# Kernel optimization log

Measured on AMD Instinct MI355X. Metric: run time of the kernel, lower is better.

Reference implementation:

```python
import jax, jax.numpy as jnp
import numpy as np

N_NODES = 10000
N_EDGES = 160000
DIM = 128
NLAYERS = 3
NBASIS = 16
NSPECIES = 100
CUTOFF = 5.0


def _mlp(x, W1, b1, W2, b2):
    # FullyConnectedNet([hidden, out]) with silu on hidden, linear output
    return jax.nn.silu(x @ W1 + b1) @ W2 + b2


def setup_inputs() -> dict:
    key = jax.random.key(0)
    ks = iter(jax.random.split(key, 64))
    scale = 0.08

    def w(shape):
        return jax.random.normal(next(ks), shape, dtype=jnp.float32) * scale

    inp = {
        "species": jax.random.randint(next(ks), (N_NODES,), 0, NSPECIES, dtype=jnp.int32),
        "edge_src": jnp.sort(jax.random.randint(next(ks), (N_EDGES,), 0, N_NODES, dtype=jnp.int32)),
        "edge_dst": jax.random.randint(next(ks), (N_EDGES,), 0, N_NODES, dtype=jnp.int32),
        "distances": 0.5 + 4.4 * jax.random.uniform(next(ks), (N_EDGES,), dtype=jnp.float32),
        "vec": jax.random.normal(next(ks), (N_EDGES, 3), dtype=jnp.float32),
        "switch": jax.random.uniform(next(ks), (N_EDGES,), dtype=jnp.float32),
        "species_W": w((NSPECIES, DIM)),
        "species_b": w((DIM,)),
        "radial_W": w((NLAYERS, NBASIS, DIM)),
        "radial_b": w((NLAYERS, DIM)),
    }
    for nm, out in [("a", DIM), ("F", 1), ("f", DIM), ("R", DIM), ("r", DIM), ("u", DIM)]:
        inp[nm + "_W1"] = w((NLAYERS, DIM, DIM))
        inp[nm + "_b1"] = w((NLAYERS, DIM))
        inp[nm + "_W2"] = w((NLAYERS, DIM, out))
        inp[nm + "_b2"] = w((NLAYERS, out))
    return inp


def reference(species, edge_src, edge_dst, distances, vec, switch,
              species_W, species_b, radial_W, radial_b,
              a_W1, a_b1, a_W2, a_b2,
              F_W1, F_b1, F_W2, F_b2,
              f_W1, f_b1, f_W2, f_b2,
              R_W1, R_b1, R_W2, R_b2,
              r_W1, r_b1, r_W2, r_b2,
              u_W1, u_b1, u_W2, u_b2):
    N = species.shape[0]
    # species encoding -> species_linear Dense
    xi = jax.nn.one_hot(species, NSPECIES, dtype=jnp.float32) @ species_W + species_b  # (N, dim)
    sw = switch[:, None]                                   # (E, 1)
    dirij = vec / distances[:, None] * sw                  # (E, 3)
    # gaussian radial basis on [0, cutoff]
    centers = jnp.linspace(0.0, CUTOFF, NBASIS, dtype=jnp.float32)
    eta = jnp.float32((NBASIS / CUTOFF) ** 2)
    rb = jnp.exp(-eta * (distances[:, None] - centers) ** 2)  # (E, nbasis)

    fi = None
    di = None
    for l in range(NLAYERS):
        ai = _mlp(xi, a_W1[l], a_b1[l], a_W2[l], a_b2[l])          # (N, dim)
        Dij = rb @ radial_W[l] + radial_b[l]                        # (E, dim)
        mij = ai[edge_src] * ai[edge_dst] * Dij * sw                # (E, dim)
        xi = xi + jax.ops.segment_sum(mij, edge_src, N)
        Fij = _mlp(mij, F_W1[l], F_b1[l], F_W2[l], F_b2[l]) * dirij  # (E, 3)
        fij = _mlp(mij, f_W1[l], f_b1[l], f_W2[l], f_b2[l])[:, :, None] * Fij[:, None, :]  # (E, C, 3)
        fij_sum = jax.ops.segment_sum(fij, edge_src, N)             # (N, C, 3)
        fi = fij_sum if l == 0 else fi + fij_sum
        deltai = _mlp(xi, R_W1[l], R_b1[l], R_W2[l], R_b2[l])[:, :, None] * fi  # (N, C, 3)
        if l == 0:
            di = deltai
        else:
            phi_rij = _mlp(mij, r_W1[l], r_b1[l], r_W2[l], r_b2[l])  # (E, C)
            phi_r = jax.ops.segment_sum(phi_rij * sw, edge_src, N)   # (N, C)
            di = phi_r[:, :, None] * di + deltai
        scal = jnp.sum(fi * di, axis=-1)                             # (N, C)
        dui = -_mlp(xi, u_W1[l], u_b1[l], u_W2[l], u_b2[l]) * scal   # (N, dim) since C == dim
        xi = xi + dui
    return xi
```

## Files before the change

### kernel.cpp

```cpp
#include <hip/hip_runtime.h>
#include <hip/hip_bf16.h>

#define N_NODES 10000
#define N_EDGES 160000
#define DIM     128
#define NBASIS  16
#define LDT     136
#define NFE     (N_NODES*DIM)

typedef __bf16 bf16x8 __attribute__((ext_vector_type(8)));
typedef __bf16 bf16x4 __attribute__((ext_vector_type(4)));
typedef __bf16 bf16x2 __attribute__((ext_vector_type(2)));
typedef float  f32x4  __attribute__((ext_vector_type(4)));

__device__ __forceinline__ float silu_f(float x){
  return x * (1.0f / (1.0f + __expf(-x)));
}
__device__ __forceinline__ f32x4 mfma16(bf16x8 a, bf16x8 b, f32x4 c){
  return __builtin_amdgcn_mfma_f32_16x16x32_bf16(a,b,c,0,0,0);
}


struct WPtrs { const float* p[11]; };

template<bool WITH_R>
__global__ __launch_bounds__(256,2) void mlp_layer(
    int nodeB,
    const __bf16* __restrict__ mij,
    const int*    __restrict__ esrc, const float* __restrict__ dirv,
    const __bf16* __restrict__ fW1z, const float* __restrict__ fb1,
    const __bf16* __restrict__ fW2z, const float* __restrict__ fb2,
    const __bf16* __restrict__ FW1z, const float* __restrict__ Fb1,
    const float*  __restrict__ FW2v, const float* __restrict__ Fb2,
    const __bf16* __restrict__ rW1z, const float* __restrict__ rb1,
    const __bf16* __restrict__ rW2z, const float* __restrict__ rb2,
    const float*  __restrict__ swv,
    float* __restrict__ fiG, float* __restrict__ phiG,
    const float* __restrict__ X,
    const __bf16* __restrict__ RW1z, const float* __restrict__ Rb1,
    const __bf16* __restrict__ RW2z, const float* __restrict__ Rb2,
    const __bf16* __restrict__ uW1z, const float* __restrict__ ub1,
    const __bf16* __restrict__ uW2z, const float* __restrict__ ub2,
    float* __restrict__ Rv, float* __restrict__ uv)
{
  __shared__ __bf16 sH[128*LDT];
  __shared__ __bf16 sW[2][8192];
  __shared__ int    sE[128];
  __shared__ float  sDir[128*3];
  const int tid=threadIdx.x, lane=tid&63, wv=tid>>6, l15=lane&15, quad=lane>>4;

  if ((int)blockIdx.x < nodeB){
    const long row0n = (long)blockIdx.x*64 + wv*16;
    const long rA = row0n + l15;
    const bool okA = rA < N_NODES;

    bf16x8 fa[4];
    #pragma unroll
    for (int kc=0;kc<4;kc++){
      int kb=kc*32+quad*8;
      bf16x8 a;
      #pragma unroll
      for (int i=0;i<8;i++) a[i]=(__bf16)0.f;
      if (okA){
        float4 u0 = *(const float4*)(X + rA*DIM + kb);
        float4 u1 = *(const float4*)(X + rA*DIM + kb + 4);
        a[0]=(__bf16)u0.x;a[1]=(__bf16)u0.y;a[2]=(__bf16)u0.z;a[3]=(__bf16)u0.w;
        a[4]=(__bf16)u1.x;a[5]=(__bf16)u1.y;a[6]=(__bf16)u1.z;a[7]=(__bf16)u1.w;
      }
      fa[kc]=a;
    }

    f32x4 acc[8];
    auto zacc = [&](){
      #pragma unroll
      for (int ni=0;ni<8;++ni) acc[ni]=(f32x4){0.f,0.f,0.f,0.f};
    };
    auto gemmA = [&](const __bf16* __restrict__ Wz){
      #pragma unroll
      for (int kc=0;kc<4;kc++){
        #pragma unroll
        for (int ni=0;ni<8;ni++){
          bf16x8 w = *(const bf16x8*)(Wz + (long)(kc*512 + ni*64 + lane)*8);
          acc[ni]=mfma16(w,fa[kc],acc[ni]);
        }
      }
    };
    auto gemmH = [&](const __bf16* __restrict__ Wz){
      #pragma unroll
      for (int kc=0;kc<4;kc++){
        bf16x8 h0=*(bf16x8*)&sH[(wv*16+l15)*LDT + kc*32 + quad*8];
        #pragma unroll
        for (int ni=0;ni<8;ni++){
          bf16x8 w = *(const bf16x8*)(Wz + (long)(kc*512 + ni*64 + lane)*8);
          acc[ni]=mfma16(w,h0,acc[ni]);
        }
      }
    };
    auto hEpi = [&](const float* __restrict__ b1){
      #pragma unroll
      for (int ni=0;ni<8;++ni){
        int n0 = ni*16 + quad*4;
        float4 bb = *(const float4*)(b1 + n0);
        bf16x4 h;
        h[0]=(__bf16)silu_f(acc[ni][0]+bb.x);
        h[1]=(__bf16)silu_f(acc[ni][1]+bb.y);
        h[2]=(__bf16)silu_f(acc[ni][2]+bb.z);
        h[3]=(__bf16)silu_f(acc[ni][3]+bb.w);
        *(bf16x4*)&sH[(wv*16+l15)*LDT + n0] = h;
      }
    };
    auto cStoreF = [&](const float* __restrict__ b2, float* __restrict__ Y){
      if (okA){
        #pragma unroll
        for (int ni=0;ni<8;++ni){
          int n0 = ni*16 + quad*4;
          float4 bb = *(const float4*)(b2 + n0);
          float4 o;
          o.x=acc[ni][0]+bb.x; o.y=acc[ni][1]+bb.y;
          o.z=acc[ni][2]+bb.z; o.w=acc[ni][3]+bb.w;
          *(float4*)(Y + rA*DIM + n0) = o;
        }
      }
    };

    zacc(); gemmA(RW1z); hEpi(Rb1);
    zacc(); gemmH(RW2z); cStoreF(Rb2, Rv);
    zacc(); gemmA(uW1z); hEpi(ub1);
    zacc(); gemmH(uW2z); cStoreF(ub2, uv);
    return;
  }

  const long row0 = (long)(blockIdx.x - nodeB)*128;
  const int  rloc0 = wv*32 + l15;
  const long rB0 = row0 + rloc0, rB1 = rB0+16;

  if (tid < 32)  *(int4*)&sE[tid*4]    = *(const int4*)(esrc + row0 + tid*4);
  if (tid >= 64 && tid < 160)
    *(float4*)&sDir[(tid-64)*4] = *(const float4*)(dirv + row0*3 + (tid-64)*4);

  bf16x8 fb[2][4];
  #pragma unroll
  for (int kc=0;kc<4;kc++){
    fb[0][kc] = *(const bf16x8*)(mij + rB0*DIM + kc*32 + quad*8);
    fb[1][kc] = *(const bf16x8*)(mij + rB1*DIM + kc*32 + quad*8);
  }
  float swr[2];
  if constexpr (WITH_R){ swr[0]=swv[rB0]; swr[1]=swv[rB1]; }

  f32x4 acc[2][8];
  bf16x8 pre[4];
  float eF[2];

  auto preload = [&](const __bf16* __restrict__ Wz, int half){
    #pragma unroll
    for (int it=0; it<4; ++it)
      pre[it] = *(const bf16x8*)(Wz + (long)(half*1024 + it*256 + tid)*8);
  };
  auto writePre = [&](int b){
    #pragma unroll
    for (int it=0; it<4; ++it)
      *(bf16x8*)&sW[b][(it*256+tid)*8] = pre[it];
  };
  auto zacc = [&](){
    #pragma unroll
    for (int mi=0;mi<2;++mi)
      #pragma unroll
      for (int ni=0;ni<8;++ni) acc[mi][ni]=(f32x4){0.f,0.f,0.f,0.f};
  };
  auto mfmaB = [&](int b, int half){
    #pragma unroll
    for (int k2=0;k2<2;k2++){
      int kc = half*2 + k2;
      #pragma unroll
      for (int ni=0;ni<8;ni++){
        bf16x8 w = *(bf16x8*)&sW[b][(k2*512 + ni*64 + lane)*8];
        acc[0][ni]=mfma16(w,fb[0][kc],acc[0][ni]);
        acc[1][ni]=mfma16(w,fb[1][kc],acc[1][ni]);
      }
    }
  };
  auto mfmaH = [&](int b, int half){
    #pragma unroll
    for (int k2=0;k2<2;k2++){
      int kc = half*2 + k2;
      bf16x8 h0=*(bf16x8*)&sH[(rloc0   )*LDT + kc*32 + quad*8];
      bf16x8 h1=*(bf16x8*)&sH[(rloc0+16)*LDT + kc*32 + quad*8];
      #pragma unroll
      for (int ni=0;ni<8;ni++){
        bf16x8 w = *(bf16x8*)&sW[b][(k2*512 + ni*64 + lane)*8];
        acc[0][ni]=mfma16(w,h0,acc[0][ni]);
        acc[1][ni]=mfma16(w,h1,acc[1][ni]);
      }
    }
  };
  auto fEpi = [&](){
    float fb2v = Fb2[0];
    #pragma unroll
    for (int mi=0;mi<2;++mi){
      float p = 0.f;
      #pragma unroll
      for (int ni=0;ni<8;++ni){
        int n0 = ni*16 + quad*4;
        float4 bb = *(const float4*)(Fb1 + n0);
        float4 w2 = *(const float4*)(FW2v + n0);
        p += silu_f(acc[mi][ni][0]+bb.x)*w2.x;
        p += silu_f(acc[mi][ni][1]+bb.y)*w2.y;
        p += silu_f(acc[mi][ni][2]+bb.z)*w2.z;
        p += silu_f(acc[mi][ni][3]+bb.w)*w2.w;
      }
      p += __shfl_xor(p,16);
      p += __shfl_xor(p,32);
      eF[mi] = p + fb2v;
    }
  };
  auto hEpi = [&](const float* __restrict__ b1){
    #pragma unroll
    for (int mi=0;mi<2;++mi){
      int rl = wv*32 + mi*16 + l15;
      #pragma unroll
      for (int ni=0;ni<8;++ni){
        int n0 = ni*16 + quad*4;
        float4 bb = *(const float4*)(b1 + n0);
        bf16x4 h;
        h[0]=(__bf16)silu_f(acc[mi][ni][0]+bb.x);
        h[1]=(__bf16)silu_f(acc[mi][ni][1]+bb.y);
        h[2]=(__bf16)silu_f(acc[mi][ni][2]+bb.z);
        h[3]=(__bf16)silu_f(acc[mi][ni][3]+bb.w);
        *(bf16x4*)&sH[rl*LDT + n0] = h;
      }
    }
  };
  auto outLDS = [&](const float* __restrict__ b2, const float* mul){
    #pragma unroll
    for (int mi=0;mi<2;++mi){
      int rl = wv*32 + mi*16 + l15;
      #pragma unroll
      for (int ni=0;ni<8;++ni){
        int n0 = ni*16 + quad*4;
        float4 bb = *(const float4*)(b2 + n0);
        bf16x4 o;
        o[0]=(__bf16)((acc[mi][ni][0]+bb.x)*mul[mi]);
        o[1]=(__bf16)((acc[mi][ni][1]+bb.y)*mul[mi]);
        o[2]=(__bf16)((acc[mi][ni][2]+bb.z)*mul[mi]);
        o[3]=(__bf16)((acc[mi][ni][3]+bb.w)*mul[mi]);
        *(bf16x4*)&sH[rl*LDT + n0] = o;
      }
    }
  };
  auto reduceFi = [&](){
    const int d = lane*2;
    float a0=0.f,a1=0.f,a2=0.f,a3=0.f,a4=0.f,a5=0.f;
    int cur = sE[wv*32];
    for (int i=0;i<32;i++){
      int e = wv*32+i;
      int n = sE[e];
      if (n != cur){
        long b = (long)cur*DIM + d;
        atomicAdd(&fiG[0L*NFE + b  ], a0);
        atomicAdd(&fiG[0L*NFE + b+1], a3);
        atomicAdd(&fiG[1L*NFE + b  ], a1);
        atomicAdd(&fiG[1L*NFE + b+1], a4);
        atomicAdd(&fiG[2L*NFE + b  ], a2);
        atomicAdd(&fiG[2L*NFE + b+1], a5);
        a0=a1=a2=a3=a4=a5=0.f; cur=n;
      }
      bf16x2 v = *(bf16x2*)&sH[e*LDT + d];
      float vx=(float)v[0], vy=(float)v[1];
      float d0=sDir[e*3+0], d1=sDir[e*3+1], d2=sDir[e*3+2];
      a0+=vx*d0; a1+=vx*d1; a2+=vx*d2;
      a3+=vy*d0; a4+=vy*d1; a5+=vy*d2;
    }
    long b = (long)cur*DIM + d;
    atomicAdd(&fiG[0L*NFE + b  ], a0);
    atomicAdd(&fiG[0L*NFE + b+1], a3);
    atomicAdd(&fiG[1L*NFE + b  ], a1);
    atomicAdd(&fiG[1L*NFE + b+1], a4);
    atomicAdd(&fiG[2L*NFE + b  ], a2);
    atomicAdd(&fiG[2L*NFE + b+1], a5);
  };
  auto reducePhi = [&](){
    const int d = lane*2;
    float a0=0.f,a1=0.f;
    int cur = sE[wv*32];
    for (int i=0;i<32;i++){
      int e = wv*32+i;
      int n = sE[e];
      if (n != cur){
        atomicAdd(&phiG[(long)cur*DIM + d  ], a0);
        atomicAdd(&phiG[(long)cur*DIM + d+1], a1);
        a0=a1=0.f; cur=n;
      }
      bf16x2 v = *(bf16x2*)&sH[e*LDT + d];
      a0 += (float)v[0]; a1 += (float)v[1];
    }
    atomicAdd(&phiG[(long)cur*DIM + d  ], a0);
    atomicAdd(&phiG[(long)cur*DIM + d+1], a1);
  };

  preload(FW1z,0); writePre(0);
  __syncthreads();
  preload(FW1z,1);
  zacc(); mfmaB(0,0);
  writePre(1);
  __syncthreads();
  preload(fW1z,0);
  mfmaB(1,1);
  writePre(0);
  __syncthreads();
  preload(fW1z,1);
  fEpi();
  zacc(); mfmaB(0,0);
  writePre(1);
  __syncthreads();
  preload(fW2z,0);
  mfmaB(1,1);
  writePre(0);
  __syncthreads();
  preload(fW2z,1);
  hEpi(fb1);
  zacc(); mfmaH(0,0);
  writePre(1);
  __syncthreads();
  if constexpr (WITH_R) preload(rW1z,0);
  mfmaH(1,1);
  outLDS(fb2, eF);
  reduceFi();

  if constexpr (WITH_R){
    writePre(0);
    __syncthreads();
    preload(rW1z,1);
    zacc(); mfmaB(0,0);
    writePre(1);
    __syncthreads();
    preload(rW2z,0);
    mfmaB(1,1);
    writePre(0);
    __syncthreads();
    preload(rW2z,1);
    hEpi(rb1);
    zacc(); mfmaH(0,0);
    writePre(1);
    __syncthreads();
    mfmaH(1,1);
    outLDS(rb2, swr);
    reducePhi();
  }
}

__global__ __launch_bounds__(64,4) void mlp_a(
    const float* __restrict__ X,
    const __bf16* __restrict__ W1z, const float* __restrict__ b1,
    const __bf16* __restrict__ W2z, const float* __restrict__ b2,
    __bf16* __restrict__ Y)
{
  __shared__ __bf16 sH[16*LDT];
  const int lane=threadIdx.x, l15=lane&15, quad=lane>>4;
  const long row0=(long)blockIdx.x*16;
  const long rA=row0+l15;

  bf16x8 fa[4];
  #pragma unroll
  for (int kc=0;kc<4;kc++){
    int kb=kc*32+quad*8;
    float4 u0 = *(const float4*)(X + rA*DIM + kb);
    float4 u1 = *(const float4*)(X + rA*DIM + kb + 4);
    bf16x8 a;
    a[0]=(__bf16)u0.x;a[1]=(__bf16)u0.y;a[2]=(__bf16)u0.z;a[3]=(__bf16)u0.w;
    a[4]=(__bf16)u1.x;a[5]=(__bf16)u1.y;a[6]=(__bf16)u1.z;a[7]=(__bf16)u1.w;
    fa[kc]=a;
  }

  f32x4 acc[8];
  #pragma unroll
  for (int ni=0;ni<8;++ni) acc[ni]=(f32x4){0.f,0.f,0.f,0.f};
  #pragma unroll
  for (int kc=0;kc<4;kc++){
    #pragma unroll
    for (int ni=0;ni<8;ni++){
      bf16x8 w = *(const bf16x8*)(W1z + (long)(kc*512 + ni*64 + lane)*8);
      acc[ni]=mfma16(w,fa[kc],acc[ni]);
    }
  }
  #pragma unroll
  for (int ni=0;ni<8;++ni){
    int n0 = ni*16 + quad*4;
    float4 bb = *(const float4*)(b1 + n0);
    bf16x4 h;
    h[0]=(__bf16)silu_f(acc[ni][0]+bb.x);
    h[1]=(__bf16)silu_f(acc[ni][1]+bb.y);
    h[2]=(__bf16)silu_f(acc[ni][2]+bb.z);
    h[3]=(__bf16)silu_f(acc[ni][3]+bb.w);
    *(bf16x4*)&sH[l15*LDT + n0] = h;
  }
  #pragma unroll
  for (int ni=0;ni<8;++ni) acc[ni]=(f32x4){0.f,0.f,0.f,0.f};
  #pragma unroll
  for (int kc=0;kc<4;kc++){
    bf16x8 h0=*(bf16x8*)&sH[l15*LDT + kc*32 + quad*8];
    #pragma unroll
    for (int ni=0;ni<8;ni++){
      bf16x8 w = *(const bf16x8*)(W2z + (long)(kc*512 + ni*64 + lane)*8);
      acc[ni]=mfma16(w,h0,acc[ni]);
    }
  }
  #pragma unroll
  for (int ni=0;ni<8;++ni){
    int n0 = ni*16 + quad*4;
    float4 bb = *(const float4*)(b2 + n0);
    bf16x4 o;
    o[0]=(__bf16)(acc[ni][0]+bb.x);
    o[1]=(__bf16)(acc[ni][1]+bb.y);
    o[2]=(__bf16)(acc[ni][2]+bb.z);
    o[3]=(__bf16)(acc[ni][3]+bb.w);
    *(bf16x4*)(Y + rA*DIM + n0) = o;
  }
}

__global__ __launch_bounds__(256) void setup_all(
    WPtrs wp, __bf16* __restrict__ wt,
    const int* __restrict__ species, const float* __restrict__ spW,
    const float* __restrict__ spB, float* __restrict__ xi, float* __restrict__ fi,
    float* __restrict__ phi,
    const float* __restrict__ dist, const float* __restrict__ vec,
    const float* __restrict__ swv, float* __restrict__ dir, float* __restrict__ rb)
{
  const int b = blockIdx.x, tid = threadIdx.x;
  if (b < 33){
    int t = b/3, l = b%3;
    const float* src = wp.p[t] + (size_t)l*16384;
    __bf16* out = wt + (size_t)b*16384;
    for (int it=0; it<8; ++it){
      int fi_ = it*256 + tid;
      int kc = fi_>>9, ni = (fi_>>6)&7, lane = fi_&63;
      int n  = ni*16 + (lane&15);
      int k0 = kc*32 + (lane>>4)*8;
      bf16x8 v;
      #pragma unroll
      for (int j=0;j<8;++j) v[j] = (__bf16)src[(k0+j)*DIM + n];
      *(bf16x8*)(out + (size_t)fi_*8) = v;
    }
  } else if (b < 33 + 5000){
    int idx = (b-33)*256 + tid;
    int n = idx >> 7, d = idx & 127;
    xi[idx] = spW[species[n]*DIM + d] + spB[d];
    phi[idx] = 0.f;
    fi[idx] = 0.f;
    fi[NFE + idx] = 0.f;
    fi[2L*NFE + idx] = 0.f;
  } else {
    int e = (b-5033)*256 + tid;
    if (e < N_EDGES){
      float d = dist[e];
      float s = swv[e];
      float inv = s / d;
      dir[e*3+0] = vec[e*3+0]*inv;
      dir[e*3+1] = vec[e*3+1]*inv;
      dir[e*3+2] = vec[e*3+2]*inv;
      const float eta = (16.0f/5.0f)*(16.0f/5.0f);
      #pragma unroll
      for (int j=0;j<NBASIS;j++){
        float c = (float)j * (5.0f/15.0f);
        float t2 = d - c;
        rb[e*NBASIS + j] = __expf(-eta*t2*t2);
      }
    }
  }
}

__global__ __launch_bounds__(256) void mij_segsum(
    const __bf16* __restrict__ ai, const int* __restrict__ esrc, const int* __restrict__ edst,
    const float* __restrict__ swv, const float* __restrict__ rb,
    const float* __restrict__ radW, const float* __restrict__ radB,
    __bf16* __restrict__ mij, float* __restrict__ xi)
{
  __shared__ float sRb[64*NBASIS];
  __shared__ int   sS[64], sD[64];
  __shared__ float sSw[64];
  int tid = threadIdx.x;
  int e0 = blockIdx.x * 64;
  *(float4*)(sRb + tid*4) = *(const float4*)(rb + (long)e0*NBASIS + tid*4);
  if (tid < 64){
    sS[tid]  = esrc[e0+tid];
    sD[tid]  = edst[e0+tid];
    sSw[tid] = swv[e0+tid];
  }
  const int wv = tid>>6, lane = tid&63;
  const int d = lane*2;
  float2 rw[NBASIS];
  #pragma unroll
  for (int j=0;j<NBASIS;j++)
    rw[j] = *(const float2*)(radW + j*DIM + d);
  float2 rB = *(const float2*)(radB + d);
  __syncthreads();

  float sx=0.f, sy=0.f;
  int cur = sS[wv*16];
  #pragma unroll
  for (int i=0;i<16;i++){
    int el = wv*16 + i;
    int n = sS[el];
    if (n != cur){
      atomicAdd(&xi[(long)cur*DIM+d  ], sx);
      atomicAdd(&xi[(long)cur*DIM+d+1], sy);
      sx=0.f; sy=0.f; cur=n;
    }
    bf16x2 as = *(const bf16x2*)(ai + (long)n*DIM + d);
    bf16x2 ad = *(const bf16x2*)(ai + (long)sD[el]*DIM + d);
    float acc0 = 0.f, acc1 = 0.f;
    #pragma unroll
    for (int j=0;j<NBASIS;j++){
      float rbv = sRb[el*NBASIS+j];
      acc0 += rbv*rw[j].x;
      acc1 += rbv*rw[j].y;
    }
    float sw_ = sSw[el];
    float m0 = (float)as[0]*(float)ad[0]*(acc0+rB.x)*sw_;
    float m1 = (float)as[1]*(float)ad[1]*(acc1+rB.y)*sw_;
    bf16x2 m; m[0]=(__bf16)m0; m[1]=(__bf16)m1;
    *(bf16x2*)(mij + (long)(e0+el)*DIM + d) = m;
    sx += m0; sy += m1;
  }
  atomicAdd(&xi[(long)cur*DIM+d  ], sx);
  atomicAdd(&xi[(long)cur*DIM+d+1], sy);
}

__global__ __launch_bounds__(256) void node_update(
    const float* __restrict__ Rv, const float* __restrict__ uv,
    float* __restrict__ fi, float* __restrict__ di, float* __restrict__ xi,
    float* __restrict__ phi, float* __restrict__ out, int layer)
{
  long idx = (long)blockIdx.x*256 + threadIdx.x;
  float f0 = fi[idx];
  float f1 = fi[NFE + idx];
  float f2 = fi[2L*NFE + idx];
  float phi_v = (layer > 0) ? phi[idx] : 0.f;
  float Rv_ = Rv[idx];
  float fv[3] = {f0,f1,f2};
  float sc = 0.f;
  #pragma unroll
  for (int k=0;k<3;k++){
    float delta = Rv_*fv[k];
    float dv = (layer==0) ? delta : phi_v*di[(long)k*NFE + idx] + delta;
    di[(long)k*NFE + idx] = dv;
    sc += fv[k]*dv;
  }
  float nx = xi[idx] - uv[idx]*sc;
  xi[idx] = nx;
  phi[idx] = 0.f;
  if (layer == 2) out[idx] = nx;
}

extern "C" void kernel_launch(void* const* d_in, const int* in_sizes, int n_in,
                              void* d_out, int out_size, void* d_ws, size_t ws_size,
                              hipStream_t stream) {
  const int*   species = (const int*)  d_in[0];
  const int*   esrc    = (const int*)  d_in[1];
  const int*   edst    = (const int*)  d_in[2];
  const float* dist    = (const float*)d_in[3];
  const float* vec     = (const float*)d_in[4];
  const float* swv     = (const float*)d_in[5];
  const float* spW     = (const float*)d_in[6];
  const float* spB     = (const float*)d_in[7];
  const float* radW    = (const float*)d_in[8];
  const float* radB    = (const float*)d_in[9];
  const float* aW1=(const float*)d_in[10], *aB1=(const float*)d_in[11], *aW2=(const float*)d_in[12], *aB2=(const float*)d_in[13];
  const float* FW1=(const float*)d_in[14], *FB1=(const float*)d_in[15], *FW2=(const float*)d_in[16], *FB2=(const float*)d_in[17];
  const float* fW1=(const float*)d_in[18], *fB1=(const float*)d_in[19], *fW2=(const float*)d_in[20], *fB2=(const float*)d_in[21];
  const float* RW1=(const float*)d_in[22], *RB1=(const float*)d_in[23], *RW2=(const float*)d_in[24], *RB2=(const float*)d_in[25];
  const float* rW1=(const float*)d_in[26], *rB1=(const float*)d_in[27], *rW2=(const float*)d_in[28], *rB2=(const float*)d_in[29];
  const float* uW1=(const float*)d_in[30], *uB1=(const float*)d_in[31], *uW2=(const float*)d_in[32], *uB2=(const float*)d_in[33];

  const long NF = (long)N_NODES*DIM;
  const long EF = (long)N_EDGES*DIM;
  float* ws   = (float*)d_ws;
  float* xi   = ws;
  float* Rv   = xi   + NF;
  float* uv   = Rv   + NF;
  float* phi  = uv   + NF;
  float* fi   = phi  + NF;
  float* di   = fi   + 3*NF;
  float* dir  = di   + 3*NF;
  float* rb   = dir  + 3L*N_EDGES;
  char* bp = (char*)(rb + 16L*N_EDGES);
  size_t off = ((size_t)(bp - (char*)d_ws) + 15) & ~(size_t)15;
  __bf16* ai   = (__bf16*)((char*)d_ws + off);
  __bf16* mij  = ai  + NF;
  __bf16* wt   = mij + EF;

  WPtrs wp;
  wp.p[0]=aW1; wp.p[1]=aW2; wp.p[2]=FW1; wp.p[3]=fW1; wp.p[4]=fW2;
  wp.p[5]=RW1; wp.p[6]=RW2; wp.p[7]=rW1; wp.p[8]=rW2; wp.p[9]=uW1; wp.p[10]=uW2;

  setup_all<<<5658, 256, 0, stream>>>(wp, wt,
                                      species, spW, spB, xi, fi, phi,
                                      dist, vec, swv, dir, rb);

  const int nodeB = (N_NODES + 63)/64;
  const int edgeB = N_EDGES/128;
  #define WT(t,l) (wt + (size_t)((t)*3+(l))*16384)

  for (int l=0;l<3;l++){
    const long bo = (long)l*DIM;

    mlp_a<<<N_NODES/16, 64, 0, stream>>>(xi, WT(0,l), aB1+bo, WT(1,l), aB2+bo, ai);
    mij_segsum<<<N_EDGES/64, 256, 0, stream>>>(ai, esrc, edst, swv, rb,
                                               radW + (long)l*NBASIS*DIM, radB + bo,
                                               mij, xi);
    if (l == 0)
      mlp_layer<false><<<nodeB+edgeB, 256, 0, stream>>>(
          nodeB, mij, esrc, dir,
          WT(3,l), fB1+bo, WT(4,l), fB2+bo,
          WT(2,l), FB1+bo, FW2+(long)l*DIM, FB2+l,
          nullptr, nullptr, nullptr, nullptr, nullptr,
          fi, phi,
          xi, WT(5,l), RB1+bo, WT(6,l), RB2+bo,
          WT(9,l), uB1+bo, WT(10,l), uB2+bo, Rv, uv);
    else
      mlp_layer<true><<<nodeB+edgeB, 256, 0, stream>>>(
          nodeB, mij, esrc, dir,
          WT(3,l), fB1+bo, WT(4,l), fB2+bo,
          WT(2,l), FB1+bo, FW2+(long)l*DIM, FB2+l,
          WT(7,l), rB1+bo, WT(8,l), rB2+bo, swv,
          fi, phi,
          xi, WT(5,l), RB1+bo, WT(6,l), RB2+bo,
          WT(9,l), uB1+bo, WT(10,l), uB2+bo, Rv, uv);
    node_update<<<5000, 256, 0, stream>>>(Rv, uv, fi, di, xi, phi,
                                          (float*)d_out, l);
  }
}
```

Measured before the change: 502.3 us.

## Fuse node update with next layer's atom MLP and pad direction vectors

Replaces the elementwise node_update kernel with node_upd_a, which computes the di/xi update for 16 nodes, stages the new xi in shared memory as bf16, and immediately runs the next layer's a-MLP (two MFMA GEMMs) to produce ai. This removes the separate mlp_a launch for layers 1 and 2 and one re-read of xi. Only the layer-0 mlp_a launch remains. The update work now runs on 64-thread blocks with float4 accesses. On the last layer it skips writing di and xi and zeroing phi, storing only the output. Separately, the per-edge direction array in shared memory is padded to float4 so the reduction loop reads it with a single vector load.

```diff
diff --git a/kernel.cpp b/kernel.cpp
--- a/kernel.cpp
+++ b/kernel.cpp
@@ -46,7 +46,7 @@
   __shared__ __bf16 sH[128*LDT];
   __shared__ __bf16 sW[2][8192];
   __shared__ int    sE[128];
-  __shared__ float  sDir[128*3];
+  __shared__ float  sDir[128*4];
   const int tid=threadIdx.x, lane=tid&63, wv=tid>>6, l15=lane&15, quad=lane>>4;
 
   if ((int)blockIdx.x < nodeB){
@@ -134,9 +134,13 @@
   const int  rloc0 = wv*32 + l15;
   const long rB0 = row0 + rloc0, rB1 = rB0+16;
 
-  if (tid < 32)  *(int4*)&sE[tid*4]    = *(const int4*)(esrc + row0 + tid*4);
-  if (tid >= 64 && tid < 160)
-    *(float4*)&sDir[(tid-64)*4] = *(const float4*)(dirv + row0*3 + (tid-64)*4);
+  if (tid < 32)  *(int4*)&sE[tid*4] = *(const int4*)(esrc + row0 + tid*4);
+  if (tid >= 128){
+    int t = tid - 128;
+    long e3 = (row0 + t)*3;
+    float d0 = dirv[e3+0], d1 = dirv[e3+1], d2 = dirv[e3+2];
+    *(float4*)&sDir[t*4] = (float4){d0,d1,d2,0.f};
+  }
 
   bf16x8 fb[2][4];
   #pragma unroll
@@ -266,9 +270,9 @@
       }
       bf16x2 v = *(bf16x2*)&sH[e*LDT + d];
       float vx=(float)v[0], vy=(float)v[1];
-      float d0=sDir[e*3+0], d1=sDir[e*3+1], d2=sDir[e*3+2];
-      a0+=vx*d0; a1+=vx*d1; a2+=vx*d2;
-      a3+=vy*d0; a4+=vy*d1; a5+=vy*d2;
+      float4 dv = *(float4*)&sDir[e*4];
+      a0+=vx*dv.x; a1+=vx*dv.y; a2+=vx*dv.z;
+      a3+=vy*dv.x; a4+=vy*dv.y; a5+=vy*dv.z;
     }
     long b = (long)cur*DIM + d;
     atomicAdd(&fiG[0L*NFE + b  ], a0);
@@ -417,6 +421,119 @@
   }
 }
 
+__global__ __launch_bounds__(64,4) void node_upd_a(
+    const float* __restrict__ Rv, const float* __restrict__ uv,
+    const float* __restrict__ fi, float* __restrict__ di,
+    float* __restrict__ xi, float* __restrict__ phi,
+    float* __restrict__ out,
+    const __bf16* __restrict__ W1z, const float* __restrict__ b1,
+    const __bf16* __restrict__ W2z, const float* __restrict__ b2,
+    __bf16* __restrict__ ai, int layer)
+{
+  __shared__ __bf16 sH[16*LDT];
+  const int lane=threadIdx.x, l15=lane&15, quad=lane>>4;
+  const long base=(long)blockIdx.x*2048;
+
+  for (int j=0;j<8;++j){
+    const long idx = base + j*256 + lane*4;
+    float4 f0 = *(const float4*)(fi + idx);
+    float4 f1 = *(const float4*)(fi + NFE + idx);
+    float4 f2 = *(const float4*)(fi + 2L*NFE + idx);
+    float4 Rq = *(const float4*)(Rv + idx);
+    float4 uq = *(const float4*)(uv + idx);
+    float4 xq = *(const float4*)(xi + idx);
+    float4 ph=(float4){0,0,0,0}, e0=ph, e1=ph, e2=ph;
+    if (layer > 0){
+      ph = *(const float4*)(phi + idx);
+      e0 = *(const float4*)(di + idx);
+      e1 = *(const float4*)(di + NFE + idx);
+      e2 = *(const float4*)(di + 2L*NFE + idx);
+    }
+    float4 nd0, nd1, nd2, nx;
+    #pragma unroll
+    for (int c=0;c<4;++c){
+      float d0v = ((const float*)&ph)[c]*((const float*)&e0)[c]
+                + ((const float*)&Rq)[c]*((const float*)&f0)[c];
+      float d1v = ((const float*)&ph)[c]*((const float*)&e1)[c]
+                + ((const float*)&Rq)[c]*((const float*)&f1)[c];
+      float d2v = ((const float*)&ph)[c]*((const float*)&e2)[c]
+                + ((const float*)&Rq)[c]*((const float*)&f2)[c];
+      float sc = ((const float*)&f0)[c]*d0v + ((const float*)&f1)[c]*d1v
+               + ((const float*)&f2)[c]*d2v;
+      ((float*)&nd0)[c]=d0v; ((float*)&nd1)[c]=d1v; ((float*)&nd2)[c]=d2v;
+      ((float*)&nx)[c] = ((const float*)&xq)[c] - ((const float*)&uq)[c]*sc;
+    }
+    if (layer == 2){
+      *(float4*)(out + idx) = nx;
+    } else {
+      *(float4*)(di + idx)          = nd0;
+      *(float4*)(di + NFE + idx)    = nd1;
+      *(float4*)(di + 2L*NFE + idx) = nd2;
+      *(float4*)(xi + idx) = nx;
+      if (layer > 0) *(float4*)(phi + idx) = (float4){0,0,0,0};
+      int row = j*2 + (lane>>5);
+      int col = (lane*4) & 127;
+      bf16x4 h;
+      h[0]=(__bf16)nx.x; h[1]=(__bf16)nx.y;
+      h[2]=(__bf16)nx.z; h[3]=(__bf16)nx.w;
+      *(bf16x4*)&sH[row*LDT + col] = h;
+    }
+  }
+
+  if (layer < 2){
+    bf16x8 fa[4];
+    #pragma unroll
+    for (int kc=0;kc<4;kc++)
+      fa[kc] = *(bf16x8*)&sH[l15*LDT + kc*32 + quad*8];
+
+    f32x4 acc[8];
+    #pragma unroll
+    for (int ni=0;ni<8;++ni) acc[ni]=(f32x4){0.f,0.f,0.f,0.f};
+    #pragma unroll
+    for (int kc=0;kc<4;kc++){
+      #pragma unroll
+      for (int ni=0;ni<8;ni++){
+        bf16x8 w = *(const bf16x8*)(W1z + (long)(kc*512 + ni*64 + lane)*8);
+        acc[ni]=mfma16(w,fa[kc],acc[ni]);
+      }
+    }
+    #pragma unroll
+    for (int ni=0;ni<8;++ni){
+      int n0 = ni*16 + quad*4;
+      float4 bb = *(const float4*)(b1 + n0);
+      bf16x4 h;
+      h[0]=(__bf16)silu_f(acc[ni][0]+bb.x);
+      h[1]=(__bf16)silu_f(acc[ni][1]+bb.y);
+      h[2]=(__bf16)silu_f(acc[ni][2]+bb.z);
+      h[3]=(__bf16)silu_f(acc[ni][3]+bb.w);
+      *(bf16x4*)&sH[l15*LDT + n0] = h;
+    }
+    #pragma unroll
+    for (int ni=0;ni<8;++ni) acc[ni]=(f32x4){0.f,0.f,0.f,0.f};
+    #pragma unroll
+    for (int kc=0;kc<4;kc++){
+      bf16x8 h0=*(bf16x8*)&sH[l15*LDT + kc*32 + quad*8];
+      #pragma unroll
+      for (int ni=0;ni<8;ni++){
+        bf16x8 w = *(const bf16x8*)(W2z + (long)(kc*512 + ni*64 + lane)*8);
+        acc[ni]=mfma16(w,h0,acc[ni]);
+      }
+    }
+    const long rA = (long)blockIdx.x*16 + l15;
+    #pragma unroll
+    for (int ni=0;ni<8;++ni){
+      int n0 = ni*16 + quad*4;
+      float4 bb = *(const float4*)(b2 + n0);
+      bf16x4 o;
+      o[0]=(__bf16)(acc[ni][0]+bb.x);
+      o[1]=(__bf16)(acc[ni][1]+bb.y);
+      o[2]=(__bf16)(acc[ni][2]+bb.z);
+      o[3]=(__bf16)(acc[ni][3]+bb.w);
+      *(bf16x4*)(ai + rA*DIM + n0) = o;
+    }
+  }
+}
+
 __global__ __launch_bounds__(256) void setup_all(
     WPtrs wp, __bf16* __restrict__ wt,
     const int* __restrict__ species, const float* __restrict__ spW,
@@ -525,32 +642,6 @@
   atomicAdd(&xi[(long)cur*DIM+d+1], sy);
 }
 
-__global__ __launch_bounds__(256) void node_update(
-    const float* __restrict__ Rv, const float* __restrict__ uv,
-    float* __restrict__ fi, float* __restrict__ di, float* __restrict__ xi,
-    float* __restrict__ phi, float* __restrict__ out, int layer)
-{
-  long idx = (long)blockIdx.x*256 + threadIdx.x;
-  float f0 = fi[idx];
-  float f1 = fi[NFE + idx];
-  float f2 = fi[2L*NFE + idx];
-  float phi_v = (layer > 0) ? phi[idx] : 0.f;
-  float Rv_ = Rv[idx];
-  float fv[3] = {f0,f1,f2};
-  float sc = 0.f;
-  #pragma unroll
-  for (int k=0;k<3;k++){
-    float delta = Rv_*fv[k];
-    float dv = (layer==0) ? delta : phi_v*di[(long)k*NFE + idx] + delta;
-    di[(long)k*NFE + idx] = dv;
-    sc += fv[k]*dv;
-  }
-  float nx = xi[idx] - uv[idx]*sc;
-  xi[idx] = nx;
-  phi[idx] = 0.f;
-  if (layer == 2) out[idx] = nx;
-}
-
 extern "C" void kernel_launch(void* const* d_in, const int* in_sizes, int n_in,
                               void* d_out, int out_size, void* d_ws, size_t ws_size,
                               hipStream_t stream) {
@@ -600,10 +691,11 @@
   const int edgeB = N_EDGES/128;
   #define WT(t,l) (wt + (size_t)((t)*3+(l))*16384)
 
+  mlp_a<<<N_NODES/16, 64, 0, stream>>>(xi, WT(0,0), aB1, WT(1,0), aB2, ai);
+
   for (int l=0;l<3;l++){
     const long bo = (long)l*DIM;
 
-    mlp_a<<<N_NODES/16, 64, 0, stream>>>(xi, WT(0,l), aB1+bo, WT(1,l), aB2+bo, ai);
     mij_segsum<<<N_EDGES/64, 256, 0, stream>>>(ai, esrc, edst, swv, rb,
                                                radW + (long)l*NBASIS*DIM, radB + bo,
                                                mij, xi);
@@ -625,7 +717,9 @@
           fi, phi,
           xi, WT(5,l), RB1+bo, WT(6,l), RB2+bo,
           WT(9,l), uB1+bo, WT(10,l), uB2+bo, Rv, uv);
-    node_update<<<5000, 256, 0, stream>>>(Rv, uv, fi, di, xi, phi,
-                                          (float*)d_out, l);
+    int ln = (l < 2) ? (l+1) : 0;
+    node_upd_a<<<N_NODES/16, 64, 0, stream>>>(
+        Rv, uv, fi, di, xi, phi, (float*)d_out,
+        WT(0,ln), aB1+(long)ln*DIM, WT(1,ln), aB2+(long)ln*DIM, ai, l);
   }
 }
```

Result: faster. 490.4 us (-2.4%).
